# Kernel optimization log

Hardware: AMD Instinct MI355X
Metric: run time of the kernel (lower is better)

## Reference

```python
import jax, jax.numpy as jnp
import numpy as np

B, S, DQ, DK, H, D = 4, 2048, 1024, 1024, 16, 64


def setup_inputs() -> dict:
    key = jax.random.key(0)
    k1, k2, k3, k4 = jax.random.split(key, 4)
    # xavier_uniform bound for Linear(in, out): sqrt(6/(in+out))
    bq = float(np.sqrt(6.0 / (DQ + H * D)))
    bk = float(np.sqrt(6.0 / (DK + H * D)))
    return {
        "query_input": jax.random.normal(k1, (B, S, DQ), dtype=jnp.float32),
        "key_input": jax.random.normal(k2, (B, S, DK), dtype=jnp.float32),
        "Wq": jax.random.uniform(k3, (H * D, DQ), minval=-bq, maxval=bq, dtype=jnp.float32),
        "bq": jnp.zeros((H * D,), dtype=jnp.float32),
        "Wk": jax.random.uniform(k4, (H * D, DK), minval=-bk, maxval=bk, dtype=jnp.float32),
        "bk": jnp.zeros((H * D,), dtype=jnp.float32),
    }


def reference(query_input, key_input, Wq, bq, Wk, bk):
    scaling = D ** (-0.5)
    # projections: (B, S, H*D) -> (B, S, H, D)
    q = (query_input @ Wq.T + bq).reshape(B, S, H, D) * scaling
    k = (key_input @ Wk.T + bk).reshape(B, S, H, D)
    # scores: (B, H, S, S), softmax over keys
    scores = jnp.einsum("bqhd,bkhd->bhqk", q, k)
    attn = jax.nn.softmax(scores, axis=-1)
    # NOTE: module reuses K as the value tensor (no V projection)
    out = jnp.einsum("bhqk,bkhd->bqhd", attn, k)
    return out.reshape(B, S, H * D)
```

## Files before the change

kernel.cpp:

```cpp
#include <hip/hip_runtime.h>
#include <stdint.h>

#define NB 4
#define NS 2048
#define NH 16
#define ND 64
#define NHD 1024
#define NK 1024

typedef __attribute__((ext_vector_type(8))) short short8;
typedef __attribute__((ext_vector_type(4))) float f32x4;
typedef __attribute__((ext_vector_type(16))) float f32x16;
typedef __attribute__((ext_vector_type(4))) unsigned u32x4;

__device__ __forceinline__ unsigned short f2bf(float f) {
    union { float f; unsigned u; } v; v.f = f;
    return (unsigned short)((v.u + 0x7fffu + ((v.u >> 16) & 1u)) >> 16);
}

__device__ __forceinline__ void gload_lds16(const unsigned short* g, unsigned short* l) {
    __builtin_amdgcn_global_load_lds(
        (const __attribute__((address_space(1))) void*)g,
        (__attribute__((address_space(3))) void*)l, 16, 0, 0);
}

__device__ __forceinline__ unsigned cvtpk(float lo, float hi) {
    unsigned r;
    asm volatile("v_cvt_pk_bf16_f32 %0, %1, %2" : "=v"(r) : "v"(lo), "v"(hi));
    return r;
}
__device__ __forceinline__ void plswap(unsigned& a, unsigned& b) {
    asm volatile("v_permlane32_swap_b32 %0, %1" : "+v"(a), "+v"(b));
}
__device__ __forceinline__ float exp2_raw(float x) {
    float r;
    asm("v_exp_f32 %0, %1" : "=v"(r) : "v"(x));
    return r;
}

__global__ void cvt_w_bf16(const float* __restrict__ Wq, const float* __restrict__ Wk,
                           unsigned short* __restrict__ Wqb, unsigned short* __restrict__ Wkb) {
    const int n4 = (NK * NHD) / 4;
    const int stride = gridDim.x * blockDim.x;
    for (int i = blockIdx.x * blockDim.x + threadIdx.x; i < 2 * n4; i += stride) {
        const int m = i < n4 ? 0 : 1;
        const int j = m ? i - n4 : i;
        const float4 v = m ? ((const float4*)Wk)[j] : ((const float4*)Wq)[j];
        ushort4 o;
        o.x = f2bf(v.x); o.y = f2bf(v.y); o.z = f2bf(v.z); o.w = f2bf(v.w);
        if (m) ((ushort4*)Wkb)[j] = o; else ((ushort4*)Wqb)[j] = o;
    }
}

#define PH_SYNC() do { __builtin_amdgcn_s_barrier(); __builtin_amdgcn_sched_barrier(0); \
    asm volatile("s_waitcnt lgkmcnt(0)" ::: "memory"); __builtin_amdgcn_sched_barrier(0); } while (0)
#define PH_END()  do { __builtin_amdgcn_s_barrier(); __builtin_amdgcn_sched_barrier(0); } while (0)

#define RD_AF(MH, KK)                                                                     \
    _Pragma("unroll")                                                                     \
    for (int mi_ = 0; mi_ < 4; ++mi_) {                                                   \
        const int rowA_ = wm + (MH) * 64 + mi_ * 16 + lr;                                 \
        af[mi_] = *(const short8*)(Ab + (rowA_ << 7) + (((KK) * 64 + lg * 16) ^ swzr));   \
    }
#define RD_BF(KK)                                                                         \
    _Pragma("unroll")                                                                     \
    for (int ni_ = 0; ni_ < 4; ++ni_) {                                                   \
        const int rowB_ = wn + ni_ * 16 + lr;                                             \
        bfr[ni_] = *(const short8*)(Bb + (rowB_ << 7) + (((KK) * 64 + lg * 16) ^ swzr));  \
    }
#define DO_MFMA(MH)                                                                       \
    do {                                                                                  \
        __builtin_amdgcn_s_setprio(1);                                                    \
        _Pragma("unroll")                                                                 \
        for (int mi_ = 0; mi_ < 4; ++mi_)                                                 \
            _Pragma("unroll")                                                             \
            for (int ni_ = 0; ni_ < 4; ++ni_)                                             \
                acc[(MH) * 4 + mi_][ni_] = __builtin_amdgcn_mfma_f32_16x16x32_bf16(       \
                    af[mi_], bfr[ni_], acc[(MH) * 4 + mi_][ni_], 0, 0, 0);                \
        __builtin_amdgcn_s_setprio(0);                                                    \
    } while (0)

__global__ __launch_bounds__(512, 2) void proj_gemm3(
    const float* __restrict__ Xq,
    const float* __restrict__ Xk,
    const unsigned short* __restrict__ Wqb,
    const unsigned short* __restrict__ Wkb,
    const float* __restrict__ bqv,
    const float* __restrict__ bkv,
    unsigned short* __restrict__ Qo,
    unsigned short* __restrict__ Ko,
    unsigned short* __restrict__ KTo,
    float qscale)
{
    extern __shared__ __attribute__((aligned(16))) char smem[];

    const int bid = blockIdx.x;
    const int wg = (bid & 7) * 32 + (bid >> 3);
    const int mp = wg >> 2;
    const int nb = wg & 3;
    const int which = mp >> 5;
    const long bm = (long)(mp & 31) * 256;
    const long bn = (long)nb * 256;

    const float* A32         = which ? Xk : Xq;
    const unsigned short* Wt = which ? Wkb : Wqb;
    const float* bias        = which ? bkv : bqv;
    unsigned short* outp     = which ? Ko : Qo;
    unsigned short* outT     = which ? KTo : nullptr;
    const float scale        = which ? 1.0f : qscale;

    const int t = threadIdx.x;
    const int lane = t & 63;
    const int w = t >> 6;
    const int wm = (w >> 2) * 128, wn = (w & 3) * 64;
    const int lr = lane & 15, lg = lane >> 4;
    const int swzr = (lr & 7) << 4;

    f32x4 acc[8][4];
    #pragma unroll
    for (int i = 0; i < 8; ++i)
        #pragma unroll
        for (int jj = 0; jj < 4; ++jj) acc[i][jj] = (f32x4){0.f, 0.f, 0.f, 0.f};

    float4 aset[8];

    auto LOADA = [&](int k0) {
        #pragma unroll
        for (int c = 0; c < 4; ++c) {
            const int u2 = c * 512 + t;
            const int row = u2 >> 3, c8 = u2 & 7;
            const float* src = A32 + (bm + row) * (long)NK + k0 + c8 * 8;
            aset[2 * c]     = *(const float4*)src;
            aset[2 * c + 1] = *(const float4*)(src + 4);
        }
    };
    auto WRITEA = [&](int buf) {
        char* Ad = smem + buf * 32768;
        #pragma unroll
        for (int c = 0; c < 4; ++c) {
            const int u2 = c * 512 + t;
            const int row = u2 >> 3;
            const int cbyte = ((u2 & 7) << 4) ^ ((row & 7) << 4);
            u32x4 wv;
            wv[0] = cvtpk(aset[2 * c].x, aset[2 * c].y);
            wv[1] = cvtpk(aset[2 * c].z, aset[2 * c].w);
            wv[2] = cvtpk(aset[2 * c + 1].x, aset[2 * c + 1].y);
            wv[3] = cvtpk(aset[2 * c + 1].z, aset[2 * c + 1].w);
            *(u32x4*)(Ad + (row << 7) + cbyte) = wv;
        }
    };
    const int scolB = (((lane & 7) ^ (lane >> 3)) << 3);
    auto BGLOAD = [&](int k0, int buf) {
        unsigned short* Bd = (unsigned short*)(smem + 65536 + buf * 32768);
        #pragma unroll
        for (int c = 0; c < 4; ++c) {
            const int rowB = c * 64 + w * 8 + (lane >> 3);
            gload_lds16(Wt + (bn + rowB) * (long)NK + k0 + scolB,
                        Bd + (size_t)(c * 64 + w * 8) * 64);
        }
    };

    BGLOAD(0, 0);
    asm volatile("" ::: "memory");
    LOADA(0);
    asm volatile("" ::: "memory");
    WRITEA(0);
    __builtin_amdgcn_sched_barrier(0);
    LOADA(64);
    asm volatile("s_waitcnt lgkmcnt(0)" ::: "memory");
    __builtin_amdgcn_s_barrier();
    __builtin_amdgcn_sched_barrier(0);

    for (int it = 0; it < 16; ++it) {
        const int cur = it & 1;
        const char* Ab = (const char*)smem + cur * 32768;
        const char* Bb = (const char*)smem + 65536 + cur * 32768;
        short8 af[4], bfr[4];

        RD_BF(0); RD_AF(0, 0);
        if (it + 1 < 16) BGLOAD((it + 1) * 64, cur ^ 1);
        PH_SYNC(); DO_MFMA(0); PH_END();

        RD_AF(1, 0);
        if (it + 1 < 16) WRITEA(cur ^ 1);
        PH_SYNC(); DO_MFMA(1); PH_END();

        RD_BF(1); RD_AF(0, 1);
        if (it + 2 < 16) LOADA((it + 2) * 64);
        PH_SYNC(); DO_MFMA(0); PH_END();

        RD_AF(1, 1);
        if (it + 2 < 16)      asm volatile("s_waitcnt vmcnt(20)" ::: "memory");
        else if (it + 1 < 16) asm volatile("s_waitcnt vmcnt(0)" ::: "memory");
        PH_SYNC(); DO_MFMA(1); PH_END();
    }

    const int h = (int)((bn + wn) >> 6);
    float bvv[4];
    #pragma unroll
    for (int ni = 0; ni < 4; ++ni) bvv[ni] = bias[(int)bn + wn + ni * 16 + lr];
    #pragma unroll
    for (int mi = 0; mi < 8; ++mi) {
        const int m0 = (int)bm + wm + mi * 16 + lg * 4;
        const int b = m0 >> 11, s0 = m0 & 2047;
        unsigned short vv[4][4];
        #pragma unroll
        for (int ni = 0; ni < 4; ++ni)
            #pragma unroll
            for (int r = 0; r < 4; ++r)
                vv[ni][r] = f2bf((acc[mi][ni][r] + bvv[ni]) * scale);
        unsigned short* orow = outp + (((size_t)(b * NH + h)) * NS + s0) * ND;
        #pragma unroll
        for (int r = 0; r < 4; ++r)
            #pragma unroll
            for (int ni = 0; ni < 4; ++ni)
                orow[(size_t)r * ND + ni * 16 + lr] = vv[ni][r];
        if (outT) {
            #pragma unroll
            for (int ni = 0; ni < 4; ++ni) {
                const int d = ni * 16 + lr;
                ushort4 tv; tv.x = vv[ni][0]; tv.y = vv[ni][1]; tv.z = vv[ni][2]; tv.w = vv[ni][3];
                *(ushort4*)&outT[(((size_t)(b * NH + h)) * ND + d) * NS + s0] = tv;
            }
        }
    }
}

#define PACK_P(s0, s1, paw, lsum)                                              \
    do {                                                                       \
        _Pragma("unroll")                                                      \
        for (int tt_ = 0; tt_ < 2; ++tt_) {                                    \
            unsigned c_[8];                                                    \
            _Pragma("unroll")                                                  \
            for (int j_ = 0; j_ < 8; ++j_) {                                   \
                const float plo_ = exp2_raw(tt_ ? s1[2 * j_]     : s0[2 * j_]);   \
                const float phi_ = exp2_raw(tt_ ? s1[2 * j_ + 1] : s0[2 * j_ + 1]); \
                (lsum) += plo_ + phi_;                                         \
                c_[j_] = cvtpk(plo_, phi_);                                    \
            }                                                                  \
            plswap(c_[0], c_[2]); plswap(c_[1], c_[3]);                        \
            plswap(c_[4], c_[6]); plswap(c_[5], c_[7]);                        \
            paw[2 * tt_]     = (u32x4){c_[0], c_[1], c_[2], c_[3]};            \
            paw[2 * tt_ + 1] = (u32x4){c_[4], c_[5], c_[6], c_[7]};            \
        }                                                                      \
    } while (0)

__global__ __launch_bounds__(512, 4) void attn_fused(
    const unsigned short* __restrict__ Qb,
    const unsigned short* __restrict__ Kb,
    const unsigned short* __restrict__ KTb,
    float* __restrict__ outp)
{
    __shared__ __attribute__((aligned(16))) unsigned short LDSA[2 * 4 * 4096];

    const int t = threadIdx.x;
    const int lane = t & 63;
    const int wq = t >> 6;
    const int q5 = lane & 31;
    const int hi = lane >> 5;

    const int Bid = blockIdx.x + 8 * blockIdx.y + 128 * blockIdx.z;
    const int xcd = Bid & 7;
    const int wIdx = Bid >> 3;
    const int qblk = wIdx & 7;
    const int g = xcd * 8 + (wIdx >> 3);
    const int h = g & 15, b = g >> 4;
    const int qbase = qblk * 256 + wq * 32;

    const unsigned short* Qh  = Qb  + ((size_t)(b * NH + h)) * NS * ND;
    const unsigned short* Kh  = Kb  + ((size_t)(b * NH + h)) * NS * ND;
    const unsigned short* KTh = KTb + ((size_t)(b * NH + h)) * ND * NS;

    short8 qB[4];
    {
        const unsigned short* Qrow = Qh + (size_t)(qbase + q5) * ND;
        #pragma unroll
        for (int kd = 0; kd < 4; ++kd)
            qB[kd] = *(const short8*)&Qrow[kd * 16 + hi * 8];
    }

    const int srow = wq * 8 + (lane >> 3);
    const int scol = ((((lane & 7) << 4) ^ ((srow & 7) << 4)) >> 1);

    f32x16 acc0, acc1;
    float l_run = 0.f;
    #pragma unroll
    for (int r = 0; r < 16; ++r) { acc0[r] = 0.f; acc1[r] = 0.f; }

    const int swz = (q5 & 7) << 4;
    const int ro0 = q5 * 128, ro1 = ro0 + 4096;

    auto STAGE = [&](int buf, int kt ) {
        unsigned short* Bd = &LDSA[buf * 16384];
        gload_lds16(Kh  + (size_t)(kt + srow) * ND + scol,        Bd         + wq * 512);
        gload_lds16(KTh + (size_t)srow * NS + kt + scol,          Bd + 4096  + wq * 512);
        gload_lds16(Kh  + (size_t)(kt + 64 + srow) * ND + scol,   Bd + 8192  + wq * 512);
        gload_lds16(KTh + (size_t)srow * NS + (kt + 64) + scol,   Bd + 12288 + wq * 512);
    };

    auto COMPUTE = [&](const char* Kbuf) {
        const char* Ktbuf = Kbuf + 8192;

        f32x16 s0, s1;
        #pragma unroll
        for (int r = 0; r < 16; ++r) { s0[r] = 0.f; s1[r] = 0.f; }
        __builtin_amdgcn_s_setprio(1);
        #pragma unroll
        for (int kd = 0; kd < 4; ++kd) {
            const int cb = (kd * 32 + hi * 16) ^ swz;
            short8 kf0 = *(const short8*)(Kbuf + ro0 + cb);
            short8 kf1 = *(const short8*)(Kbuf + ro1 + cb);
            s0 = __builtin_amdgcn_mfma_f32_32x32x16_bf16(kf0, qB[kd], s0, 0, 0, 0);
            s1 = __builtin_amdgcn_mfma_f32_32x32x16_bf16(kf1, qB[kd], s1, 0, 0, 0);
        }
        __builtin_amdgcn_s_setprio(0);

        u32x4 paw[4];
        PACK_P(s0, s1, paw, l_run);

        __builtin_amdgcn_s_setprio(1);
        #pragma unroll
        for (int ks = 0; ks < 4; ++ks) {
            union { u32x4 u; short8 s; } pa; pa.u = paw[ks];
            const int cb = (ks * 32 + hi * 16) ^ swz;
            short8 vf0 = *(const short8*)(Ktbuf + ro0 + cb);
            short8 vf1 = *(const short8*)(Ktbuf + ro1 + cb);
            acc0 = __builtin_amdgcn_mfma_f32_32x32x16_bf16(pa.s, vf0, acc0, 0, 0, 0);
            acc1 = __builtin_amdgcn_mfma_f32_32x32x16_bf16(pa.s, vf1, acc1, 0, 0, 0);
        }
        __builtin_amdgcn_s_setprio(0);
    };

    STAGE(0, 0);
    for (int it = 0; it < NS / 128; ++it) {
        const int cur = it & 1;
        asm volatile("s_waitcnt vmcnt(0)" ::: "memory");
        __syncthreads();
        if (it < NS / 128 - 1) STAGE(cur ^ 1, (it + 1) * 128);

        const char* base = (const char*)LDSA + cur * 32768;
        COMPUTE(base);
        COMPUTE(base + 16384);
    }

    const float lt = l_run + __shfl_xor(l_run, 32);
    const float inv = 1.0f / lt;
    #pragma unroll
    for (int r = 0; r < 16; ++r) {
        const int qr = (r & 3) + 8 * (r >> 2) + 4 * hi;
        const float invr = __shfl(inv, qr);
        float* orow = outp + ((size_t)b * NS + (qbase + qr)) * NHD + h * ND;
        orow[q5]      = acc0[r] * invr;
        orow[32 + q5] = acc1[r] * invr;
    }
}

extern "C" void kernel_launch(void* const* d_in, const int* in_sizes, int n_in,
                              void* d_out, int out_size, void* d_ws, size_t ws_size,
                              hipStream_t stream) {
    const float* xq = (const float*)d_in[0];
    const float* xk = (const float*)d_in[1];
    const float* Wq = (const float*)d_in[2];
    const float* bq = (const float*)d_in[3];
    const float* Wk = (const float*)d_in[4];
    const float* bk = (const float*)d_in[5];
    float* outp = (float*)d_out;

    unsigned short* Wqb = (unsigned short*)d_ws;
    unsigned short* Wkb = Wqb + 1048576;
    unsigned short* Qb  = Wkb + 1048576;
    unsigned short* Kb  = Qb  + 8388608;
    unsigned short* KTb = Kb  + 8388608;

    static bool lds_init = false;
    if (!lds_init) {
        hipFuncSetAttribute((const void*)proj_gemm3,
                            hipFuncAttributeMaxDynamicSharedMemorySize, 131072);
        lds_init = true;
    }

    cvt_w_bf16<<<1024, 256, 0, stream>>>(Wq, Wk, Wqb, Wkb);

    const float qscale = 0.125f * 1.4426950408889634f;
    proj_gemm3<<<256, 512, 131072, stream>>>(xq, xk, Wqb, Wkb, bq, bk,
                                             Qb, Kb, KTb, qscale);

    attn_fused<<<dim3(8, 16, 4), 512, 0, stream>>>(Qb, Kb, KTb, outp);
}
```

Measured before the change: 138.3 us.

## Reshape projection GEMM tile to 128x512 to halve fp32 activation loads

Changes the projection GEMM block tile from 256x256 to 128 rows by 512 columns, so each block stages half as many fp32 activation rows and twice as many bf16 weight rows. The per-k-step schedule is reworked to split the B tile into two halves loaded in different phases, and accumulators are rearranged to 4x8 per wave. The epilogue writes two heads per wave. LDS use rises to 160KB, and waitcnt thresholds are retuned, which risks pipelining stalls.

```diff
diff --git a/kernel.cpp b/kernel.cpp
--- a/kernel.cpp
+++ b/kernel.cpp
@@ -56,31 +56,31 @@
     asm volatile("s_waitcnt lgkmcnt(0)" ::: "memory"); __builtin_amdgcn_sched_barrier(0); } while (0)
 #define PH_END()  do { __builtin_amdgcn_s_barrier(); __builtin_amdgcn_sched_barrier(0); } while (0)
 
-#define RD_AF(MH, KK)                                                                     \
+#define RD_AF(KK)                                                                         \
     _Pragma("unroll")                                                                     \
     for (int mi_ = 0; mi_ < 4; ++mi_) {                                                   \
-        const int rowA_ = wm + (MH) * 64 + mi_ * 16 + lr;                                 \
+        const int rowA_ = wm + mi_ * 16 + lr;                                             \
         af[mi_] = *(const short8*)(Ab + (rowA_ << 7) + (((KK) * 64 + lg * 16) ^ swzr));   \
     }
-#define RD_BF(KK)                                                                         \
+#define RD_BF(KK, NHF)                                                                    \
     _Pragma("unroll")                                                                     \
     for (int ni_ = 0; ni_ < 4; ++ni_) {                                                   \
-        const int rowB_ = wn + ni_ * 16 + lr;                                             \
+        const int rowB_ = wn + (NHF) * 64 + ni_ * 16 + lr;                                \
         bfr[ni_] = *(const short8*)(Bb + (rowB_ << 7) + (((KK) * 64 + lg * 16) ^ swzr));  \
     }
-#define DO_MFMA(MH)                                                                       \
+#define DO_MFMA(NHF)                                                                      \
     do {                                                                                  \
         __builtin_amdgcn_s_setprio(1);                                                    \
         _Pragma("unroll")                                                                 \
         for (int mi_ = 0; mi_ < 4; ++mi_)                                                 \
             _Pragma("unroll")                                                             \
             for (int ni_ = 0; ni_ < 4; ++ni_)                                             \
-                acc[(MH) * 4 + mi_][ni_] = __builtin_amdgcn_mfma_f32_16x16x32_bf16(       \
-                    af[mi_], bfr[ni_], acc[(MH) * 4 + mi_][ni_], 0, 0, 0);                \
+                acc[mi_][(NHF) * 4 + ni_] = __builtin_amdgcn_mfma_f32_16x16x32_bf16(      \
+                    af[mi_], bfr[ni_], acc[mi_][(NHF) * 4 + ni_], 0, 0, 0);               \
         __builtin_amdgcn_s_setprio(0);                                                    \
     } while (0)
 
-__global__ __launch_bounds__(512, 2) void proj_gemm3(
+__global__ __launch_bounds__(512, 2) void proj_gemm5(
     const float* __restrict__ Xq,
     const float* __restrict__ Xk,
     const unsigned short* __restrict__ Wqb,
@@ -96,11 +96,11 @@
 
     const int bid = blockIdx.x;
     const int wg = (bid & 7) * 32 + (bid >> 3);
-    const int mp = wg >> 2;
-    const int nb = wg & 3;
-    const int which = mp >> 5;
-    const long bm = (long)(mp & 31) * 256;
-    const long bn = (long)nb * 256;
+    const int mp = wg >> 1;
+    const int nb = wg & 1;
+    const int which = mp >> 6;
+    const long bm = (long)(mp & 63) * 128;
+    const long bn = (long)nb * 512;
 
     const float* A32         = which ? Xk : Xq;
     const unsigned short* Wt = which ? Wkb : Wqb;
@@ -112,21 +112,21 @@
     const int t = threadIdx.x;
     const int lane = t & 63;
     const int w = t >> 6;
-    const int wm = (w >> 2) * 128, wn = (w & 3) * 64;
+    const int wm = (w >> 2) * 64, wn = (w & 3) * 128;
     const int lr = lane & 15, lg = lane >> 4;
     const int swzr = (lr & 7) << 4;
 
-    f32x4 acc[8][4];
-    #pragma unroll
-    for (int i = 0; i < 8; ++i)
-        #pragma unroll
-        for (int jj = 0; jj < 4; ++jj) acc[i][jj] = (f32x4){0.f, 0.f, 0.f, 0.f};
-
-    float4 aset[8];
+    f32x4 acc[4][8];
+    #pragma unroll
+    for (int i = 0; i < 4; ++i)
+        #pragma unroll
+        for (int jj = 0; jj < 8; ++jj) acc[i][jj] = (f32x4){0.f, 0.f, 0.f, 0.f};
+
+    float4 aset[4];
 
     auto LOADA = [&](int k0) {
         #pragma unroll
-        for (int c = 0; c < 4; ++c) {
+        for (int c = 0; c < 2; ++c) {
             const int u2 = c * 512 + t;
             const int row = u2 >> 3, c8 = u2 & 7;
             const float* src = A32 + (bm + row) * (long)NK + k0 + c8 * 8;
@@ -135,9 +135,9 @@
         }
     };
     auto WRITEA = [&](int buf) {
-        char* Ad = smem + buf * 32768;
-        #pragma unroll
-        for (int c = 0; c < 4; ++c) {
+        char* Ad = smem + buf * 16384;
+        #pragma unroll
+        for (int c = 0; c < 2; ++c) {
             const int u2 = c * 512 + t;
             const int row = u2 >> 3;
             const int cbyte = ((u2 & 7) << 4) ^ ((row & 7) << 4);
@@ -150,17 +150,17 @@
         }
     };
     const int scolB = (((lane & 7) ^ (lane >> 3)) << 3);
-    auto BGLOAD = [&](int k0, int buf) {
-        unsigned short* Bd = (unsigned short*)(smem + 65536 + buf * 32768);
+    auto BGLOAD = [&](int k0, int buf, int half) {
+        unsigned short* Bd = (unsigned short*)(smem + 32768 + buf * 65536);
         #pragma unroll
         for (int c = 0; c < 4; ++c) {
-            const int rowB = c * 64 + w * 8 + (lane >> 3);
+            const int rowB = half * 256 + c * 64 + w * 8 + (lane >> 3);
             gload_lds16(Wt + (bn + rowB) * (long)NK + k0 + scolB,
-                        Bd + (size_t)(c * 64 + w * 8) * 64);
-        }
-    };
-
-    BGLOAD(0, 0);
+                        Bd + (size_t)rowB * 64);
+        }
+    };
+
+    BGLOAD(0, 0, 0); BGLOAD(0, 0, 1);
     asm volatile("" ::: "memory");
     LOADA(0);
     asm volatile("" ::: "memory");
@@ -173,55 +173,64 @@
 
     for (int it = 0; it < 16; ++it) {
         const int cur = it & 1;
-        const char* Ab = (const char*)smem + cur * 32768;
-        const char* Bb = (const char*)smem + 65536 + cur * 32768;
+        const char* Ab = (const char*)smem + cur * 16384;
+        const char* Bb = (const char*)smem + 32768 + cur * 65536;
         short8 af[4], bfr[4];
 
-        RD_BF(0); RD_AF(0, 0);
-        if (it + 1 < 16) BGLOAD((it + 1) * 64, cur ^ 1);
+        RD_BF(0, 0); RD_AF(0);
+        if (it + 1 < 16) BGLOAD((it + 1) * 64, cur ^ 1, 0);
         PH_SYNC(); DO_MFMA(0); PH_END();
 
-        RD_AF(1, 0);
+        RD_BF(0, 1);
         if (it + 1 < 16) WRITEA(cur ^ 1);
         PH_SYNC(); DO_MFMA(1); PH_END();
 
-        RD_BF(1); RD_AF(0, 1);
+        RD_BF(1, 0); RD_AF(1);
+        if (it + 1 < 16) BGLOAD((it + 1) * 64, cur ^ 1, 1);
         if (it + 2 < 16) LOADA((it + 2) * 64);
         PH_SYNC(); DO_MFMA(0); PH_END();
 
-        RD_AF(1, 1);
-        if (it + 2 < 16)      asm volatile("s_waitcnt vmcnt(20)" ::: "memory");
+        RD_BF(1, 1);
+        if (it + 2 < 16)      asm volatile("s_waitcnt vmcnt(4)" ::: "memory");
         else if (it + 1 < 16) asm volatile("s_waitcnt vmcnt(0)" ::: "memory");
         PH_SYNC(); DO_MFMA(1); PH_END();
     }
 
-    const int h = (int)((bn + wn) >> 6);
-    float bvv[4];
-    #pragma unroll
-    for (int ni = 0; ni < 4; ++ni) bvv[ni] = bias[(int)bn + wn + ni * 16 + lr];
-    #pragma unroll
-    for (int mi = 0; mi < 8; ++mi) {
+    const int h0 = (int)((bn + wn) >> 6);
+    float bvv[8];
+    #pragma unroll
+    for (int nj = 0; nj < 8; ++nj) bvv[nj] = bias[(int)bn + wn + nj * 16 + lr];
+    #pragma unroll
+    for (int mi = 0; mi < 4; ++mi) {
         const int m0 = (int)bm + wm + mi * 16 + lg * 4;
         const int b = m0 >> 11, s0 = m0 & 2047;
-        unsigned short vv[4][4];
-        #pragma unroll
-        for (int ni = 0; ni < 4; ++ni)
+        unsigned short vv[8][4];
+        #pragma unroll
+        for (int nj = 0; nj < 8; ++nj)
             #pragma unroll
             for (int r = 0; r < 4; ++r)
-                vv[ni][r] = f2bf((acc[mi][ni][r] + bvv[ni]) * scale);
-        unsigned short* orow = outp + (((size_t)(b * NH + h)) * NS + s0) * ND;
+                vv[nj][r] = f2bf((acc[mi][nj][r] + bvv[nj]) * scale);
         #pragma unroll
         for (int r = 0; r < 4; ++r)
             #pragma unroll
-            for (int ni = 0; ni < 4; ++ni)
-                orow[(size_t)r * ND + ni * 16 + lr] = vv[ni][r];
+            for (int nh = 0; nh < 2; ++nh) {
+                unsigned short* orow = outp +
+                    (((size_t)(b * NH + h0 + nh)) * NS + (s0 + r)) * ND;
+                #pragma unroll
+                for (int ni = 0; ni < 4; ++ni)
+                    orow[ni * 16 + lr] = vv[nh * 4 + ni][r];
+            }
         if (outT) {
             #pragma unroll
-            for (int ni = 0; ni < 4; ++ni) {
-                const int d = ni * 16 + lr;
-                ushort4 tv; tv.x = vv[ni][0]; tv.y = vv[ni][1]; tv.z = vv[ni][2]; tv.w = vv[ni][3];
-                *(ushort4*)&outT[(((size_t)(b * NH + h)) * ND + d) * NS + s0] = tv;
-            }
+            for (int nh = 0; nh < 2; ++nh)
+                #pragma unroll
+                for (int ni = 0; ni < 4; ++ni) {
+                    const int d = ni * 16 + lr;
+                    const int nj = nh * 4 + ni;
+                    ushort4 tv; tv.x = vv[nj][0]; tv.y = vv[nj][1];
+                    tv.z = vv[nj][2]; tv.w = vv[nj][3];
+                    *(ushort4*)&outT[(((size_t)(b * NH + h0 + nh)) * ND + d) * NS + s0] = tv;
+                }
         }
     }
 }
@@ -374,15 +383,15 @@
 
     static bool lds_init = false;
     if (!lds_init) {
-        hipFuncSetAttribute((const void*)proj_gemm3,
-                            hipFuncAttributeMaxDynamicSharedMemorySize, 131072);
+        hipFuncSetAttribute((const void*)proj_gemm5,
+                            hipFuncAttributeMaxDynamicSharedMemorySize, 163840);
         lds_init = true;
     }
 
     cvt_w_bf16<<<1024, 256, 0, stream>>>(Wq, Wk, Wqb, Wkb);
 
     const float qscale = 0.125f * 1.4426950408889634f;
-    proj_gemm3<<<256, 512, 131072, stream>>>(xq, xk, Wqb, Wkb, bq, bk,
+    proj_gemm5<<<256, 512, 163840, stream>>>(xq, xk, Wqb, Wkb, bq, bk,
                                              Qb, Kb, KTb, qscale);
 
     attn_fused<<<dim3(8, 16, 4), 512, 0, stream>>>(Qb, Kb, KTb, outp);
```

After: 141.8 us. +2.5%, slower.
